# Kernel tuning notes

Hardware: AMD Instinct MI355X
Metric: run time of the kernel (lower is better)

The kernel has to match this reference:

```python
import jax, jax.numpy as jnp
import numpy as np

DT, TAU = 0.02, 0.1


def setup_inputs() -> dict:
    key = jax.random.key(0)
    ks = jax.random.split(key, 7)
    B, T, IN, H = 64, 2048, 64, 256
    return {
        "x0": jax.random.normal(ks[0], (B, H), jnp.float32),
        "I": jax.random.normal(ks[1], (B, T, IN), jnp.float32),
        "W_in": jax.random.normal(ks[2], (H, IN), jnp.float32) / np.sqrt(IN),
        "W_rec": jax.random.normal(ks[3], (H, H), jnp.float32) / np.sqrt(H),
        "b": jax.random.normal(ks[4], (H,), jnp.float32) * 0.1,
        "Wout": jax.random.normal(ks[5], (2, H), jnp.float32) / np.sqrt(H),
        "bout": jax.random.normal(ks[6], (2,), jnp.float32) * 0.1,
    }


def reference(x0, I, W_in, W_rec, b, Wout, bout):
    # Continuous-time leaky RNN, forward-Euler integration.
    # u_{t+1} = (1 - dt/tau) * u_t + (dt/tau) * (tanh(u_t) @ W_rec^T + I_t @ W_in^T + b)
    alpha = DT / TAU

    def step(u, I_t):
        r = jnp.tanh(u)                                   # [B, H]
        drive = r @ W_rec.T + I_t @ W_in.T + b            # [B, H]
        u_new = (1.0 - alpha) * u + alpha * drive
        return u_new, u_new

    I_tbf = jnp.swapaxes(I, 0, 1)                         # [T, B, IN]
    _, us = jax.lax.scan(step, x0, I_tbf)                 # [T, B, H]
    u = jnp.swapaxes(us, 0, 1)                            # [B, T, H]
    y = u @ Wout.T + bout                                 # [B, T, 2] linear readout
    return u, y
```

## Files before the change

### kernel.cpp

```cpp
#include <hip/hip_runtime.h>

#define BB 64
#define TT 2048
#define INW 64
#define HH 256
#define NXB 512
#define RPB ((BB * TT) / NXB)

typedef float v2f __attribute__((ext_vector_type(2)));

__device__ __forceinline__ v2f fma2(v2f a, v2f b, v2f c) {
#if __has_builtin(__builtin_elementwise_fma)
    return __builtin_elementwise_fma(a, b, c);
#else
    v2f r; r.x = __builtin_fmaf(a.x, b.x, c.x); r.y = __builtin_fmaf(a.y, b.y, c.y); return r;
#endif
}

__device__ __forceinline__ float fast_tanh(float x) {
    float e = __expf(2.0f * x);
    return 1.0f - 2.0f / (e + 1.0f);
}

__device__ __forceinline__ void lds_barrier() {
    asm volatile("s_waitcnt lgkmcnt(0)" ::: "memory");
    __builtin_amdgcn_s_barrier();
    __builtin_amdgcn_sched_barrier(0);
}

__global__ __launch_bounds__(256)
void xprep(const float* __restrict__ I,
           const float* __restrict__ W_in,
           const float* __restrict__ bias,
           float* __restrict__ X)
{
    const int h = threadIdx.x;
    const size_t row0 = (size_t)blockIdx.x * RPB;

    v2f w[32];
    {
        const float4* wp = (const float4*)(W_in + (size_t)h * INW);
        #pragma unroll
        for (int i = 0; i < 16; ++i) {
            float4 a = wp[i];
            w[2*i]     = (v2f){a.x, a.y};
            w[2*i + 1] = (v2f){a.z, a.w};
        }
    }
    const float bv = bias[h];

    for (int r = 0; r < RPB; ++r) {
        const float4* ip = (const float4*)(I + (row0 + r) * INW);
        v2f acc0 = {0.f, 0.f}, acc1 = {0.f, 0.f};
        #pragma unroll
        for (int i = 0; i < 16; ++i) {
            float4 iv = ip[i];
            acc0 = fma2(w[2*i],     (v2f){iv.x, iv.y}, acc0);
            acc1 = fma2(w[2*i + 1], (v2f){iv.z, iv.w}, acc1);
        }
        v2f s = acc0 + acc1;
        X[(row0 + r) * HH + h] = s.x + s.y + bv;
    }
}

__global__ __launch_bounds__(1024, 4)
void rnn_scan(const float* __restrict__ x0,
              const float* __restrict__ W_rec,
              float* uX)
{
    __shared__ __align__(16) float r_buf[HH];
    __shared__ __align__(16) float xbuf[2][HH];
    __shared__ float part[8][HH + 8];

    const int b   = blockIdx.x;
    const int tid = threadIdx.x;
    const int h2  = tid & 127;
    const int q   = tid >> 7;
    const int k0  = q * 32;
    const int hA  = h2;
    const int hB  = h2 + 128;
    const int il  = tid - 256;

    v2f wrA[16], wrB[16];
    {
        const float4* wa = (const float4*)(W_rec + (size_t)hA * HH + k0);
        const float4* wb = (const float4*)(W_rec + (size_t)hB * HH + k0);
        #pragma unroll
        for (int i = 0; i < 8; ++i) {
            float4 a = wa[i], bq = wb[i];
            wrA[2*i]     = (v2f){a.x, a.y};   wrA[2*i + 1] = (v2f){a.z, a.w};
            wrB[2*i]     = (v2f){bq.x, bq.y}; wrB[2*i + 1] = (v2f){bq.z, bq.w};
        }
    }

    float u = 0.0f;
    if (tid < HH) {
        u = x0[(size_t)b * HH + tid];
        r_buf[tid] = fast_tanh(u);
    }
    if (tid < 64)
        ((float4*)&xbuf[0][0])[tid] = ((const float4*)(uX + (size_t)b * TT * HH))[tid];
    float4 x_next = {0.f, 0.f, 0.f, 0.f};
    if ((unsigned)il < 64u)
        x_next = ((const float4*)(uX + ((size_t)b * TT + 1) * HH))[il];
    __syncthreads();

    const float4* rb4 = (const float4*)&r_buf[k0];

    for (int t = 0; t < TT; ++t) {
        float4 x_fut = {0.f, 0.f, 0.f, 0.f};
        if ((unsigned)il < 64u && (t + 2) < TT)
            x_fut = ((const float4*)(uX + ((size_t)b * TT + t + 2) * HH))[il];

        v2f aA0 = {0.f,0.f}, aA1 = {0.f,0.f}, aB0 = {0.f,0.f}, aB1 = {0.f,0.f};
        #pragma unroll
        for (int i = 0; i < 8; ++i) {
            float4 r4 = rb4[i];
            v2f r01 = (v2f){r4.x, r4.y}, r23 = (v2f){r4.z, r4.w};
            aA0 = fma2(wrA[2*i],     r01, aA0);
            aA1 = fma2(wrA[2*i + 1], r23, aA1);
            aB0 = fma2(wrB[2*i],     r01, aB0);
            aB1 = fma2(wrB[2*i + 1], r23, aB1);
        }
        v2f sA = aA0 + aA1, sB = aB0 + aB1;
        part[q][hA] = sA.x + sA.y;
        part[q][hB] = sB.x + sB.y;
        lds_barrier();

        if (tid < HH) {
            float d = (((part[0][tid] + part[1][tid]) + (part[2][tid] + part[3][tid])) +
                       ((part[4][tid] + part[5][tid]) + (part[6][tid] + part[7][tid])))
                      + xbuf[t & 1][tid];
            u = 0.8f * u + 0.2f * d;
            uX[((size_t)b * TT + t) * HH + tid] = u;
            r_buf[tid] = fast_tanh(u);
        }
        if ((unsigned)il < 64u && (t + 1) < TT)
            *(float4*)&xbuf[(t + 1) & 1][4 * il] = x_next;
        x_next = x_fut;
        lds_barrier();
    }
}

__global__ __launch_bounds__(256)
void readout(const float* __restrict__ u,
             const float* __restrict__ Wout,
             const float* __restrict__ bout,
             float* __restrict__ y)
{
    const int wid  = threadIdx.x >> 6;
    const int lane = threadIdx.x & 63;
    const size_t row = (size_t)blockIdx.x * 4 + wid;

    float4 uv = ((const float4*)(u + row * HH))[lane];
    float4 w0 = ((const float4*)Wout)[lane];
    float4 w1 = ((const float4*)(Wout + HH))[lane];

    float acc0 = uv.x * w0.x + uv.y * w0.y + uv.z * w0.z + uv.w * w0.w;
    float acc1 = uv.x * w1.x + uv.y * w1.y + uv.z * w1.z + uv.w * w1.w;

    #pragma unroll
    for (int m = 32; m >= 1; m >>= 1) {
        acc0 += __shfl_xor(acc0, m, 64);
        acc1 += __shfl_xor(acc1, m, 64);
    }
    if (lane == 0) {
        y[row * 2 + 0] = acc0 + bout[0];
        y[row * 2 + 1] = acc1 + bout[1];
    }
}

extern "C" void kernel_launch(void* const* d_in, const int* in_sizes, int n_in,
                              void* d_out, int out_size, void* d_ws, size_t ws_size,
                              hipStream_t stream) {
    const float* x0    = (const float*)d_in[0];
    const float* I     = (const float*)d_in[1];
    const float* W_in  = (const float*)d_in[2];
    const float* W_rec = (const float*)d_in[3];
    const float* bias  = (const float*)d_in[4];
    const float* Wout  = (const float*)d_in[5];
    const float* bout  = (const float*)d_in[6];

    float* u_out = (float*)d_out;
    float* y_out = u_out + (size_t)BB * TT * HH;

    xprep<<<NXB, 256, 0, stream>>>(I, W_in, bias, u_out);
    rnn_scan<<<BB, 1024, 0, stream>>>(x0, W_rec, u_out);
    readout<<<(BB * TT) / 4, 256, 0, stream>>>(u_out, Wout, bout, y_out);
}
```

Before: 1.683 ms.

## Halve scan block to 512 threads with 4 hidden outputs per thread

Reworks the recurrent matvec split so each of 8 wavefronts covers a 32-wide K chunk and each lane computes 4 consecutive hidden units. Partial sums go to LDS with one float4 store. Fewer threads per block should make each per-step barrier cheaper and reduce LDS reads of r_buf per FMA. In exchange each thread holds 128 weight floats in registers and does twice the FMA work serially.

```diff
diff --git a/kernel.cpp b/kernel.cpp
--- a/kernel.cpp
+++ b/kernel.cpp
@@ -6,6 +6,9 @@
 #define HH 256
 #define NXB 512
 #define RPB ((BB * TT) / NXB)
+#define NW 8
+#define KC (HH / NW)
+#define PSTR 260
 
 typedef float v2f __attribute__((ext_vector_type(2)));
 
@@ -63,33 +66,32 @@
     }
 }
 
-__global__ __launch_bounds__(1024, 4)
+__global__ __launch_bounds__(512, 1)
 void rnn_scan(const float* __restrict__ x0,
               const float* __restrict__ W_rec,
               float* uX)
 {
     __shared__ __align__(16) float r_buf[HH];
     __shared__ __align__(16) float xbuf[2][HH];
-    __shared__ float part[8][HH + 8];
+    __shared__ __align__(16) float part[NW][PSTR];
 
-    const int b   = blockIdx.x;
-    const int tid = threadIdx.x;
-    const int h2  = tid & 127;
-    const int q   = tid >> 7;
-    const int k0  = q * 32;
-    const int hA  = h2;
-    const int hB  = h2 + 128;
-    const int il  = tid - 256;
+    const int b    = blockIdx.x;
+    const int tid  = threadIdx.x;
+    const int lane = tid & 63;
+    const int w    = tid >> 6;
+    const int k0   = w * KC;
+    const int h0   = lane * 4;
+    const int il   = tid - 256;
 
-    v2f wrA[16], wrB[16];
-    {
-        const float4* wa = (const float4*)(W_rec + (size_t)hA * HH + k0);
-        const float4* wb = (const float4*)(W_rec + (size_t)hB * HH + k0);
+    v2f wr[4][16];
+    #pragma unroll
+    for (int m = 0; m < 4; ++m) {
+        const float4* wp = (const float4*)(W_rec + (size_t)(h0 + m) * HH + k0);
         #pragma unroll
         for (int i = 0; i < 8; ++i) {
-            float4 a = wa[i], bq = wb[i];
-            wrA[2*i]     = (v2f){a.x, a.y};   wrA[2*i + 1] = (v2f){a.z, a.w};
-            wrB[2*i]     = (v2f){bq.x, bq.y}; wrB[2*i + 1] = (v2f){bq.z, bq.w};
+            float4 a = wp[i];
+            wr[m][2*i]     = (v2f){a.x, a.y};
+            wr[m][2*i + 1] = (v2f){a.z, a.w};
         }
     }
 
@@ -112,19 +114,24 @@
         if ((unsigned)il < 64u && (t + 2) < TT)
             x_fut = ((const float4*)(uX + ((size_t)b * TT + t + 2) * HH))[il];
 
-        v2f aA0 = {0.f,0.f}, aA1 = {0.f,0.f}, aB0 = {0.f,0.f}, aB1 = {0.f,0.f};
+        v2f a0[4] = {{0.f,0.f},{0.f,0.f},{0.f,0.f},{0.f,0.f}};
+        v2f a1[4] = {{0.f,0.f},{0.f,0.f},{0.f,0.f},{0.f,0.f}};
         #pragma unroll
         for (int i = 0; i < 8; ++i) {
             float4 r4 = rb4[i];
             v2f r01 = (v2f){r4.x, r4.y}, r23 = (v2f){r4.z, r4.w};
-            aA0 = fma2(wrA[2*i],     r01, aA0);
-            aA1 = fma2(wrA[2*i + 1], r23, aA1);
-            aB0 = fma2(wrB[2*i],     r01, aB0);
-            aB1 = fma2(wrB[2*i + 1], r23, aB1);
+            #pragma unroll
+            for (int m = 0; m < 4; ++m) {
+                a0[m] = fma2(wr[m][2*i],     r01, a0[m]);
+                a1[m] = fma2(wr[m][2*i + 1], r23, a1[m]);
+            }
         }
-        v2f sA = aA0 + aA1, sB = aB0 + aB1;
-        part[q][hA] = sA.x + sA.y;
-        part[q][hB] = sB.x + sB.y;
+        float4 dv;
+        { v2f s = a0[0] + a1[0]; dv.x = s.x + s.y; }
+        { v2f s = a0[1] + a1[1]; dv.y = s.x + s.y; }
+        { v2f s = a0[2] + a1[2]; dv.z = s.x + s.y; }
+        { v2f s = a0[3] + a1[3]; dv.w = s.x + s.y; }
+        *(float4*)&part[w][h0] = dv;
         lds_barrier();
 
         if (tid < HH) {
@@ -185,6 +192,6 @@
     float* y_out = u_out + (size_t)BB * TT * HH;
 
     xprep<<<NXB, 256, 0, stream>>>(I, W_in, bias, u_out);
-    rnn_scan<<<BB, 1024, 0, stream>>>(x0, W_rec, u_out);
+    rnn_scan<<<BB, 512, 0, stream>>>(x0, W_rec, u_out);
     readout<<<(BB * TT) / 4, 256, 0, stream>>>(u_out, Wout, bout, y_out);
 }
```

New measurement: 1.761 ms. 1.05x slower.
